# Kernel tuning notes

Hardware: AMD Instinct MI355X
Metric: run time of the kernel (lower is better)

The kernel has to match this reference:

```python
import jax, jax.numpy as jnp
import numpy as np

# Mamba2 config (matches mamba_ssm.Mamba2 defaults used by the wrapper)
D_MODEL = 1024
D_STATE = 128
D_CONV = 4
EXPAND = 2
HEADDIM = 64
CHUNK = 256
D_INNER = EXPAND * D_MODEL            # 2048
NHEADS = D_INNER // HEADDIM           # 32
CONV_DIM = D_INNER + 2 * D_STATE      # 2304 (x, B, C share the causal conv)
D_IN_PROJ = 2 * D_INNER + 2 * D_STATE + NHEADS  # z, xBC, dt
EPS = 1e-5


def rmsnorm(x, w, eps=EPS):
    return x * jax.lax.rsqrt(jnp.mean(x * x, axis=-1, keepdims=True) + eps) * w


def setup_inputs() -> dict:
    key = jax.random.key(0)
    ks = jax.random.split(key, 8)
    B, L = 2, 2048
    def w(k, shape, sc=0.02):
        return jax.random.normal(k, shape, jnp.float32) * sc
    return {
        "x": jax.random.normal(ks[0], (B, L, D_MODEL), jnp.float32),
        "norm_w": jnp.ones((D_MODEL,), jnp.float32),
        "in_proj_w": w(ks[1], (D_IN_PROJ, D_MODEL)),
        "conv_w": w(ks[2], (CONV_DIM, 1, D_CONV), 0.2),   # depthwise kernel
        "conv_b": jnp.zeros((CONV_DIM,), jnp.float32),
        "dt_bias": w(ks[3], (NHEADS,), 1.0),
        "A_log": jnp.log(1.0 + 15.0 * jax.random.uniform(ks[4], (NHEADS,), jnp.float32)),
        "D": jnp.ones((NHEADS,), jnp.float32),
        "gnorm_w": jnp.ones((D_INNER,), jnp.float32),
        "out_proj_w": w(ks[5], (D_MODEL, D_INNER)),
    }


def _ssd(xd, a, Bm, Cm):
    """Chunked SSD scan (ssd_minimal_discrete).
    xd: (b,l,h,p) = x*dt ; a: (b,l,h) = dt*A ; Bm,Cm: (b,l,n) (ngroups=1)."""
    b, l, h, p = xd.shape
    n = Bm.shape[-1]
    nc = l // CHUNK
    xd = xd.reshape(b, nc, CHUNK, h, p)
    a = a.reshape(b, nc, CHUNK, h).transpose(0, 3, 1, 2)   # (b,h,nc,c)
    Bm = Bm.reshape(b, nc, CHUNK, n)
    Cm = Cm.reshape(b, nc, CHUNK, n)
    a_cs = jnp.cumsum(a, axis=-1)                           # (b,h,nc,c)
    # 1) intra-chunk: causal decay matrix L[t,s] = exp(sum_{s<i<=t} a_i)
    diff = a_cs[..., :, None] - a_cs[..., None, :]          # (b,h,nc,c,c)
    mask = jnp.tril(jnp.ones((CHUNK, CHUNK), bool))
    Lm = jnp.exp(jnp.where(mask, diff, 0.0)) * mask
    Y_diag = jnp.einsum("bcln,bcsn,bhcls,bcshp->bclhp", Cm, Bm, Lm, xd)
    # 2) per-chunk end states
    decay_states = jnp.exp(a_cs[..., -1:] - a_cs)           # (b,h,nc,c)
    states = jnp.einsum("bcln,bhcl,bclhp->bchpn", Bm, decay_states, xd)
    # 3) inter-chunk recurrence (vectorized segsum over the 8+1 chunk totals)
    tot = jnp.pad(a_cs[..., -1], ((0, 0), (0, 0), (1, 0)))  # (b,h,nc+1)
    tot_cs = jnp.cumsum(tot, axis=-1)
    dchunk = tot_cs[..., :, None] - tot_cs[..., None, :]    # (b,h,nc+1,nc+1)
    cmask = jnp.tril(jnp.ones((nc + 1, nc + 1), bool))
    dchunk = jnp.exp(jnp.where(cmask, dchunk, 0.0)) * cmask
    states = jnp.concatenate([jnp.zeros_like(states[:, :1]), states], axis=1)
    new_states = jnp.einsum("bhzc,bchpn->bzhpn", dchunk, states)
    init_states = new_states[:, :-1]                        # state entering each chunk
    # 4) state -> output contribution
    Y_off = jnp.einsum("bcln,bchpn,bhcl->bclhp", Cm, init_states, jnp.exp(a_cs))
    return (Y_diag + Y_off).reshape(b, l, h, p)


def reference(x, norm_w, in_proj_w, conv_w, conv_b, dt_bias, A_log, D, gnorm_w, out_proj_w):
    res = x
    u = rmsnorm(x, norm_w)
    zxbcdt = u @ in_proj_w.T                                # (b,l,d_in_proj)
    z, xBC, dt = jnp.split(zxbcdt, [D_INNER, D_INNER + CONV_DIM], axis=-1)
    # causal depthwise conv1d over (x,B,C), then SiLU
    xBC_t = jnp.pad(xBC.transpose(0, 2, 1), ((0, 0), (0, 0), (D_CONV - 1, 0)))
    conv = jax.lax.conv_general_dilated(
        xBC_t, conv_w, (1,), "VALID",
        dimension_numbers=("NCH", "OIH", "NCH"), feature_group_count=CONV_DIM)
    xBC = jax.nn.silu(conv.transpose(0, 2, 1) + conv_b)
    xs, Bm, Cm = jnp.split(xBC, [D_INNER, D_INNER + D_STATE], axis=-1)
    dt = jax.nn.softplus(dt + dt_bias)                      # (b,l,h)
    A = -jnp.exp(A_log)                                     # (h,)
    xh = xs.reshape(xs.shape[0], xs.shape[1], NHEADS, HEADDIM)
    y = _ssd(xh * dt[..., None], dt * A, Bm, Cm)
    y = y + D[None, None, :, None] * xh                     # skip term
    y = y.reshape(xs.shape)
    y = rmsnorm(y * jax.nn.silu(z), gnorm_w)                # gated RMSNorm
    return res + y @ out_proj_w.T
```

## Files before the change

kernel.cpp:

```cpp
#include <hip/hip_runtime.h>
#include <hip/hip_bf16.h>

typedef __hip_bfloat16 bf16_t;
typedef __attribute__((ext_vector_type(8))) short bfrag8;
typedef __attribute__((ext_vector_type(4))) float floatx4;

#define DM     1024
#define DI     2048
#define NHD    32
#define HD     64
#define DSTATE 128
#define CONVD  2304
#define NPROJ  4384
#define NPAD   4480
#define MR     4096
#define LL     2048
#define EPSF   1e-5f
#define PSTR   40
#define LOG2E  1.44269504088896f

__device__ __forceinline__ void gl_lds16(const void* g, void* l) {
  __builtin_amdgcn_global_load_lds((const __attribute__((address_space(1))) void*)g,
                                   (__attribute__((address_space(3))) void*)l, 16, 0, 0);
}
__device__ __forceinline__ unsigned pack_bf16_rn(float a, float b) {
  unsigned ua = (__float_as_uint(a) + 0x8000u) >> 16;
  unsigned ub = (__float_as_uint(b) + 0x8000u) >> 16;
  return ua | (ub << 16);
}
__device__ __forceinline__ unsigned short bf16u(float a) {
  return (unsigned short)((__float_as_uint(a) + 0x8000u) >> 16);
}
__device__ __forceinline__ float blo(unsigned u){ return __uint_as_float(u << 16); }
__device__ __forceinline__ float bhi(unsigned u){ return __uint_as_float(u & 0xffff0000u); }
__device__ __forceinline__ void unp8(uint4 u, float* v) {
  v[0]=blo(u.x); v[1]=bhi(u.x); v[2]=blo(u.y); v[3]=bhi(u.y);
  v[4]=blo(u.z); v[5]=bhi(u.z); v[6]=blo(u.w); v[7]=bhi(u.w);
}

__global__ void rms1_kernel(const float* __restrict__ x, const float* __restrict__ w,
                            bf16_t* __restrict__ ub) {
  int row = blockIdx.x, t = threadIdx.x;
  float4 v = ((const float4*)(x + (long)row * DM))[t];
  float ss = v.x*v.x + v.y*v.y + v.z*v.z + v.w*v.w;
#pragma unroll
  for (int off = 32; off > 0; off >>= 1) ss += __shfl_down(ss, off, 64);
  __shared__ float red[4];
  if ((t & 63) == 0) red[t >> 6] = ss;
  __syncthreads();
  float tot = red[0] + red[1] + red[2] + red[3];
  float rs = rsqrtf(tot * (1.f / DM) + EPSF);
  float4 wv = ((const float4*)w)[t];
  bf16_t* o = ub + (long)row * DM + t * 4;
  o[0] = __float2bfloat16(v.x * rs * wv.x);
  o[1] = __float2bfloat16(v.y * rs * wv.y);
  o[2] = __float2bfloat16(v.z * rs * wv.z);
  o[3] = __float2bfloat16(v.w * rs * wv.w);
}

#define W1CNT (NPAD * DM / 4)
#define W2CNT (DM * DI / 4)
__global__ void cvtw_kernel(const float* __restrict__ w1, const float* __restrict__ w2,
                            bf16_t* __restrict__ o1, bf16_t* __restrict__ o2) {
  int i4 = blockIdx.x * 256 + threadIdx.x;
  if (i4 < W1CNT) {
    int idx = i4 * 4;
    int row = idx >> 10;
    float4 v = make_float4(0.f, 0.f, 0.f, 0.f);
    if (row < NPROJ) v = *(const float4*)(w1 + idx);
    bf16_t* d = o1 + idx;
    d[0] = __float2bfloat16(v.x); d[1] = __float2bfloat16(v.y);
    d[2] = __float2bfloat16(v.z); d[3] = __float2bfloat16(v.w);
  } else {
    int idx = (i4 - W1CNT) * 4;
    float4 v = *(const float4*)(w2 + idx);
    bf16_t* d = o2 + idx;
    d[0] = __float2bfloat16(v.x); d[1] = __float2bfloat16(v.y);
    d[2] = __float2bfloat16(v.z); d[3] = __float2bfloat16(v.w);
  }
}

template<int TN, bool DO_RES, bool OUT_BF16>
__global__ __launch_bounds__(256) void gemm64_kernel(const bf16_t* __restrict__ A,
    const bf16_t* __restrict__ Bw, const float* __restrict__ resid,
    void* __restrict__ Cout, int N, int K) {
  __shared__ bf16_t As[128 * 64];
  __shared__ bf16_t Bs[TN * 64];
  const int tid = threadIdx.x;
  const int lane = tid & 63;
  const int wv = tid >> 6;
  const int l15 = lane & 15;
  const int l4 = lane >> 4;
  constexpr int MF = (TN == 128) ? 4 : 2;
  const int wm = (TN == 128) ? ((wv >> 1) << 6) : (wv << 5);
  const int wn = (TN == 128) ? ((wv & 1) << 6) : 0;
  const int tm = blockIdx.x << 7;
  const int tn = blockIdx.y * TN;

  floatx4 acc[MF][4];
#pragma unroll
  for (int i = 0; i < MF; i++)
#pragma unroll
    for (int j = 0; j < 4; j++) acc[i][j] = (floatx4){0.f, 0.f, 0.f, 0.f};

  const int r = tid >> 3;
  const int c8 = tid & 7;
  const int scol = ((c8 ^ (r & 7)) << 3);
  const bf16_t* Ag = A + (long)(tm + r) * K + scol;
  const bf16_t* Bg = Bw + (long)(tn + r) * K + scol;
  const int swz = l15 & 7;

  for (int k0 = 0; k0 < K; k0 += 64) {
#pragma unroll
    for (int q = 0; q < 4; q++)
      gl_lds16(Ag + (long)(q * 32) * K + k0, &As[q * 2048 + tid * 8]);
#pragma unroll
    for (int q = 0; q < TN / 32; q++)
      gl_lds16(Bg + (long)(q * 32) * K + k0, &Bs[q * 2048 + tid * 8]);
    __syncthreads();
#pragma unroll
    for (int kk = 0; kk < 2; kk++) {
      bfrag8 af[MF], bfr[4];
      const int ch = ((kk << 2) | l4) ^ swz;
#pragma unroll
      for (int j = 0; j < 4; j++)
        bfr[j] = *(const bfrag8*)&Bs[(wn + j * 16 + l15) * 64 + ch * 8];
#pragma unroll
      for (int i = 0; i < MF; i++)
        af[i] = *(const bfrag8*)&As[(wm + i * 16 + l15) * 64 + ch * 8];
#pragma unroll
      for (int i = 0; i < MF; i++)
#pragma unroll
        for (int j = 0; j < 4; j++)
          acc[i][j] = __builtin_amdgcn_mfma_f32_16x16x32_bf16(af[i], bfr[j], acc[i][j], 0, 0, 0);
    }
    __syncthreads();
  }
#pragma unroll
  for (int i = 0; i < MF; i++)
#pragma unroll
    for (int j = 0; j < 4; j++)
#pragma unroll
      for (int r2 = 0; r2 < 4; r2++) {
        int row = tm + wm + i * 16 + l4 * 4 + r2;
        int col = tn + wn + j * 16 + l15;
        float v = acc[i][j][r2];
        if (OUT_BF16) {
          ((bf16_t*)Cout)[(long)row * N + col] = __float2bfloat16(v);
        } else {
          if (DO_RES) v += resid[(long)row * N + col];
          ((float*)Cout)[(long)row * N + col] = v;
        }
      }
}

__global__ __launch_bounds__(256) void gemm_s_kernel(const bf16_t* __restrict__ Cmh,
                const bf16_t* __restrict__ Bmh, float* __restrict__ SL) {
  __shared__ bf16_t As[128 * 32];
  __shared__ bf16_t Bs[128 * 32];
  const int tid = threadIdx.x;
  const int lane = tid & 63;
  const int wv = tid >> 6;
  const int wm = (wv >> 1) << 6;
  const int wn = (wv & 1) << 6;
  const int bc = blockIdx.z;
  const int tm = blockIdx.x << 7;
  const int tn = blockIdx.y << 7;
  const int l15 = lane & 15;
  const int l4 = lane >> 4;
  floatx4 acc[4][4];
#pragma unroll
  for (int i = 0; i < 4; i++)
#pragma unroll
    for (int j = 0; j < 4; j++) acc[i][j] = (floatx4){0.f, 0.f, 0.f, 0.f};
  const int arow = tid >> 2;
  const int acol = (tid & 3) << 3;
  const bf16_t* Ag = Cmh + (long)bc * 256 * DSTATE + (long)(tm + arow) * DSTATE + acol;
  const bf16_t* Bg = Bmh + (long)bc * 256 * DSTATE + (long)(tn + arow) * DSTATE + acol;
  const long k64 = (long)64 * DSTATE;
  for (int k0 = 0; k0 < DSTATE; k0 += 32) {
    gl_lds16(Ag + k0, &As[tid * 8]);
    gl_lds16(Ag + k64 + k0, &As[2048 + tid * 8]);
    gl_lds16(Bg + k0, &Bs[tid * 8]);
    gl_lds16(Bg + k64 + k0, &Bs[2048 + tid * 8]);
    __syncthreads();
    bfrag8 af[4], bfr[4];
#pragma unroll
    for (int i = 0; i < 4; i++)
      af[i] = *(const bfrag8*)&As[(wm + i * 16 + l15) * 32 + l4 * 8];
#pragma unroll
    for (int j = 0; j < 4; j++)
      bfr[j] = *(const bfrag8*)&Bs[(wn + j * 16 + l15) * 32 + l4 * 8];
#pragma unroll
    for (int i = 0; i < 4; i++)
#pragma unroll
      for (int j = 0; j < 4; j++)
        acc[i][j] = __builtin_amdgcn_mfma_f32_16x16x32_bf16(af[i], bfr[j], acc[i][j], 0, 0, 0);
    __syncthreads();
  }
  float* Cb = SL + (long)bc * 65536;
#pragma unroll
  for (int i = 0; i < 4; i++)
#pragma unroll
    for (int j = 0; j < 4; j++)
#pragma unroll
      for (int r = 0; r < 4; r++)
        Cb[(long)(tm + wm + i * 16 + l4 * 4 + r) * 256 + tn + wn + j * 16 + l15] = acc[i][j][r];
}

__global__ __launch_bounds__(256) void conv4_kernel(const bf16_t* __restrict__ zxh,
    const float* __restrict__ cw, const float* __restrict__ cb,
    bf16_t* __restrict__ xhb, bf16_t* __restrict__ Bmh, bf16_t* __restrict__ Cmh) {
  int g = blockIdx.x * 256 + threadIdx.x;
  int cg = g % 288;
  int blt = g / 288;
  int c0 = cg * 8;
  long bl0 = (long)blt * 4;
  int l0 = (int)(bl0 & (LL - 1));
  const bf16_t* base = zxh + bl0 * NPAD + DI + c0;
  float rv[7][8];
#pragma unroll
  for (int j = 0; j < 7; j++) {
    int dj = j - 3;
    if (l0 + dj >= 0) {
      uint4 u = *(const uint4*)(base + (long)dj * NPAD);
      unp8(u, rv[j]);
    } else {
#pragma unroll
      for (int q = 0; q < 8; q++) rv[j][q] = 0.f;
    }
  }
  float4 wq[8];
#pragma unroll
  for (int q = 0; q < 8; q++) wq[q] = ((const float4*)cw)[c0 + q];
  float bias[8];
  *(float4*)&bias[0] = *(const float4*)(cb + c0);
  *(float4*)&bias[4] = *(const float4*)(cb + c0 + 4);
#pragma unroll
  for (int i = 0; i < 4; i++) {
    unsigned o[4];
#pragma unroll
    for (int q2 = 0; q2 < 4; q2++) {
      float rr[2];
#pragma unroll
      for (int e = 0; e < 2; e++) {
        int q = q2 * 2 + e;
        float a = bias[q] + wq[q].x * rv[i][q] + wq[q].y * rv[i + 1][q]
                + wq[q].z * rv[i + 2][q] + wq[q].w * rv[i + 3][q];
        rr[e] = a / (1.f + __expf(-a));
      }
      o[q2] = pack_bf16_rn(rr[0], rr[1]);
    }
    uint4 ov = make_uint4(o[0], o[1], o[2], o[3]);
    long bl = bl0 + i;
    if (c0 < DI)               *(uint4*)(xhb + bl * DI + c0) = ov;
    else if (c0 < DI + DSTATE) *(uint4*)(Bmh + bl * DSTATE + (c0 - DI)) = ov;
    else                       *(uint4*)(Cmh + bl * DSTATE + (c0 - DI - DSTATE)) = ov;
  }
}

__global__ void acs_kernel(const bf16_t* __restrict__ zxh, const float* __restrict__ A_log,
                           const float* __restrict__ dtb,
                           float* __restrict__ acs, float* __restrict__ ctot,
                           float* __restrict__ dtout) {
  int blk = blockIdx.x;
  int h = blk & 31, bc = blk >> 5;
  int t = threadIdx.x, lane = t & 63, w = t >> 6;
  float Ah = -__expf(A_log[h]) * LOG2E;
  int gl = bc * 256 + t;
  float vv = __bfloat162float(zxh[(long)gl * NPAD + (NPROJ - 32) + h]) + dtb[h];
  float sp = fmaxf(vv, 0.f) + log1pf(__expf(-fabsf(vv)));
  dtout[gl * 32 + h] = sp;
  float a = sp * Ah;
#pragma unroll
  for (int off = 1; off < 64; off <<= 1) {
    float v = __shfl_up(a, off, 64);
    if (lane >= off) a += v;
  }
  __shared__ float wsum[4];
  if (lane == 63) wsum[w] = a;
  __syncthreads();
  float base = 0.f;
  for (int i = 0; i < 4; i++) base += (i < w) ? wsum[i] : 0.f;
  a += base;
  acs[blk * 256 + t] = a;
  if (t == 255) ctot[blk] = a;
}

__global__ __launch_bounds__(256) void xdt_kernel(const bf16_t* __restrict__ xhb,
    const bf16_t* __restrict__ Bmh, const float* __restrict__ dt,
    const float* __restrict__ acs, bf16_t* __restrict__ xdT,
    bf16_t* __restrict__ xdTe, bf16_t* __restrict__ BmT) {
  __shared__ unsigned short Tb[9216];
  int blk = blockIdx.x;
  int t = threadIdx.x;
  if (blk < 512) {
    unsigned short* T1 = Tb;
    unsigned short* T2 = Tb + 4608;
    int h = blk & 31, bc = blk >> 5;
    float atot = acs[blk * 256 + 255];
    int l_loc = t >> 2, pg = t & 3;
    for (int lt = 0; lt < 4; lt++) {
      int gl = bc * 256 + lt * 64 + l_loc;
      float w1 = dt[gl * 32 + h];
      float w2 = w1 * exp2f(atot - acs[blk * 256 + lt * 64 + l_loc]);
      const uint4* src = (const uint4*)(xhb + (long)gl * DI + h * HD + pg * 16);
      uint4 u0 = src[0], u1 = src[1];
      float v[16];
      unp8(u0, v); unp8(u1, v + 8);
      __syncthreads();
#pragma unroll
      for (int q = 0; q < 16; q++) {
        T1[(pg * 16 + q) * 72 + l_loc] = bf16u(v[q] * w1);
        T2[(pg * 16 + q) * 72 + l_loc] = bf16u(v[q] * w2);
      }
      __syncthreads();
      long orow = ((long)blk * 64 + l_loc) * 256 + lt * 64 + pg * 16;
      *(uint4*)(xdT + orow)      = *(uint4*)&T1[l_loc * 72 + pg * 16];
      *(uint4*)(xdT + orow + 8)  = *(uint4*)&T1[l_loc * 72 + pg * 16 + 8];
      *(uint4*)(xdTe + orow)     = *(uint4*)&T2[l_loc * 72 + pg * 16];
      *(uint4*)(xdTe + orow + 8) = *(uint4*)&T2[l_loc * 72 + pg * 16 + 8];
    }
  } else {
    unsigned short* T = Tb;
    int bc = blk - 512;
    int l_loc = t >> 2, ng = t & 3;
    for (int lt = 0; lt < 4; lt++) {
      int gl = bc * 256 + lt * 64 + l_loc;
      const uint4* src = (const uint4*)(Bmh + (long)gl * DSTATE + ng * 32);
      uint4 u[4];
#pragma unroll
      for (int q = 0; q < 4; q++) u[q] = src[q];
      __syncthreads();
      const unsigned short* us = (const unsigned short*)u;
#pragma unroll
      for (int e = 0; e < 32; e++)
        T[(ng * 32 + e) * 72 + l_loc] = us[e];
      __syncthreads();
      int n = t >> 1, lg2 = t & 1;
      long orow = ((long)bc * 128 + n) * 256 + lt * 64 + lg2 * 32;
#pragma unroll
      for (int q = 0; q < 4; q++)
        *(uint4*)(BmT + orow + q * 8) = *(uint4*)&T[n * 72 + lg2 * 32 + q * 8];
    }
  }
}

__global__ __launch_bounds__(256) void states3_kernel(const bf16_t* __restrict__ xdTe,
    const bf16_t* __restrict__ BmT, bf16_t* __restrict__ states) {
  int blk = blockIdx.x;
  int bc = blk >> 5;
  int t = threadIdx.x, lane = t & 63, wv = t >> 6;
  int l15 = lane & 15, l4 = lane >> 4;
  floatx4 acc[2][4];
#pragma unroll
  for (int i = 0; i < 2; i++)
#pragma unroll
    for (int j = 0; j < 4; j++) acc[i][j] = (floatx4){0.f, 0.f, 0.f, 0.f};
  const bf16_t* arow = BmT + (long)bc * 128 * 256;
  const bf16_t* brow = xdTe + (long)blk * 64 * 256;
#pragma unroll
  for (int kt = 0; kt < 8; kt++) {
    bfrag8 af[2], bfr[4];
#pragma unroll
    for (int i = 0; i < 2; i++)
      af[i] = *(const bfrag8*)(arow + (long)(wv * 32 + i * 16 + l15) * 256 + kt * 32 + l4 * 8);
#pragma unroll
    for (int j = 0; j < 4; j++)
      bfr[j] = *(const bfrag8*)(brow + (long)(j * 16 + l15) * 256 + kt * 32 + l4 * 8);
#pragma unroll
    for (int i = 0; i < 2; i++)
#pragma unroll
      for (int j = 0; j < 4; j++)
        acc[i][j] = __builtin_amdgcn_mfma_f32_16x16x32_bf16(af[i], bfr[j], acc[i][j], 0, 0, 0);
  }
#pragma unroll
  for (int i = 0; i < 2; i++)
#pragma unroll
    for (int j = 0; j < 4; j++) {
      int n_base = wv * 32 + i * 16 + l4 * 4;
      int p = j * 16 + l15;
      unsigned lo = pack_bf16_rn(acc[i][j][0], acc[i][j][1]);
      unsigned hi = pack_bf16_rn(acc[i][j][2], acc[i][j][3]);
      *(uint2*)(states + (long)blk * 8192 + p * 128 + n_base) = make_uint2(lo, hi);
    }
}

__global__ void scan_kernel(const bf16_t* __restrict__ states, const float* __restrict__ ctot,
                            bf16_t* __restrict__ initsb) {
  int id = blockIdx.x * 256 + threadIdx.x;
  int pn = id & 8191;
  int bh = id >> 13;
  int b = bh >> 5, h = bh & 31;
  float S = 0.f;
#pragma unroll
  for (int c = 0; c < 8; c++) {
    int blk = (b * 8 + c) * 32 + h;
    initsb[(long)blk * 8192 + pn] = __float2bfloat16(S);
    S = exp2f(ctot[blk]) * S + __bfloat162float(states[(long)blk * 8192 + pn]);
  }
}

__global__ __launch_bounds__(256) void yk3_kernel(const float* __restrict__ SL,
     const bf16_t* __restrict__ Cmh, const bf16_t* __restrict__ xhb,
     const bf16_t* __restrict__ zxh, const float* __restrict__ acs,
     const bf16_t* __restrict__ initsb, const bf16_t* __restrict__ xdT,
     const float* __restrict__ Dp, bf16_t* __restrict__ yg, float* __restrict__ ssqp) {
  int bi = blockIdx.x;
  int mh = bi & 1, h = (bi >> 1) & 31, bc = bi >> 6;
  int ablk = bc * 32 + h;
  int t = threadIdx.x;
  int lane = t & 63, wv = t >> 6;
  int l15 = lane & 15, l4 = lane >> 4;
  __shared__ float acsS[256];
  __shared__ bf16_t Ps[128 * PSTR];
  __shared__ __align__(16) char bbuf[49152];
  bf16_t* xds = (bf16_t*)bbuf;
  bf16_t* ins = (bf16_t*)(bbuf + 32768);
  float* Yt = (float*)bbuf;

  {
    const bf16_t* xrow_g = xdT + (long)ablk * 64 * 256;
#pragma unroll
    for (int it = 0; it < 8; it++) {
      int sl = it * 256 + t;
      int p = sl >> 5, s = sl & 31;
      int c = (s & 24) | ((s & 7) ^ (p & 7));
      gl_lds16(xrow_g + p * 256 + c * 8, &xds[sl * 8]);
    }
    const bf16_t* irow_g = initsb + (long)ablk * 8192;
#pragma unroll
    for (int it = 0; it < 4; it++) {
      int sl = it * 256 + t;
      int p = sl >> 4, s = sl & 15;
      int c = (s & 8) | ((s & 7) ^ (p & 7));
      gl_lds16(irow_g + p * 128 + c * 8, &ins[sl * 8]);
    }
  }
  acsS[t] = acs[ablk * 256 + t];
  __syncthreads();

  const int l_loc = t >> 1, half = t & 1;
  const int l = mh * 128 + l_loc;
  const float al = acsS[l];
  const float eAl = exp2f(al);
  const int rowbase = bc * 256;
  const float* SLb = SL + (long)bc * 65536 + (long)l * 256;

  floatx4 acc[2][4];
#pragma unroll
  for (int i = 0; i < 2; i++)
#pragma unroll
    for (int j = 0; j < 4; j++) acc[i][j] = (floatx4){0.f, 0.f, 0.f, 0.f};

  const int nkd = (mh + 1) * 4;
  float4 slv[4];
#pragma unroll
  for (int q = 0; q < 4; q++) slv[q] = ((const float4*)(SLb + half * 16))[q];

  for (int kt = 0; kt < nkd + 4; kt++) {
    unsigned pk[8];
    if (kt < nkd) {
      int s0 = kt * 32 + half * 16;
#pragma unroll
      for (int q = 0; q < 4; q++) {
        float4 v = slv[q];
        int sb = s0 + q * 4;
        float p0 = (sb + 0 <= l) ? v.x * exp2f(al - acsS[sb + 0]) : 0.f;
        float p1 = (sb + 1 <= l) ? v.y * exp2f(al - acsS[sb + 1]) : 0.f;
        float p2 = (sb + 2 <= l) ? v.z * exp2f(al - acsS[sb + 2]) : 0.f;
        float p3 = (sb + 3 <= l) ? v.w * exp2f(al - acsS[sb + 3]) : 0.f;
        pk[q * 2 + 0] = pack_bf16_rn(p0, p1);
        pk[q * 2 + 1] = pack_bf16_rn(p2, p3);
      }
    } else {
      int n0 = (kt - nkd) * 32;
      const uint4* Cg = (const uint4*)(Cmh + (long)(rowbase + l) * DSTATE + n0 + half * 16);
      uint4 u0 = Cg[0], u1 = Cg[1];
      float cv[16];
      unp8(u0, cv); unp8(u1, cv + 8);
#pragma unroll
      for (int q = 0; q < 8; q++)
        pk[q] = pack_bf16_rn(cv[q * 2] * eAl, cv[q * 2 + 1] * eAl);
    }
    {
      uint4* pw = (uint4*)&Ps[l_loc * PSTR + half * 16];
      pw[0] = make_uint4(pk[0], pk[1], pk[2], pk[3]);
      pw[1] = make_uint4(pk[4], pk[5], pk[6], pk[7]);
    }
    if (kt + 1 < nkd) {
#pragma unroll
      for (int q = 0; q < 4; q++)
        slv[q] = ((const float4*)(SLb + (kt + 1) * 32 + half * 16))[q];
    }
    __syncthreads();
    bfrag8 bfr[4];
    if (kt < nkd) {
      int ch = kt * 4 + l4;
#pragma unroll
      for (int j = 0; j < 4; j++) {
        int p = j * 16 + l15;
        int sw = (ch & 24) | ((ch & 7) ^ (p & 7));
        bfr[j] = *(const bfrag8*)&xds[(p * 32 + sw) * 8];
      }
    } else {
      int ch = (kt - nkd) * 4 + l4;
#pragma unroll
      for (int j = 0; j < 4; j++) {
        int p = j * 16 + l15;
        int sw = (ch & 8) | ((ch & 7) ^ (p & 7));
        bfr[j] = *(const bfrag8*)&ins[(p * 16 + sw) * 8];
      }
    }
#pragma unroll
    for (int i = 0; i < 2; i++) {
      bfrag8 af = *(const bfrag8*)&Ps[(wv * 32 + i * 16 + l15) * PSTR + l4 * 8];
#pragma unroll
      for (int j = 0; j < 4; j++)
        acc[i][j] = __builtin_amdgcn_mfma_f32_16x16x32_bf16(af, bfr[j], acc[i][j], 0, 0, 0);
    }
    __syncthreads();
  }
#pragma unroll
  for (int i = 0; i < 2; i++)
#pragma unroll
    for (int j = 0; j < 4; j++)
#pragma unroll
      for (int r = 0; r < 4; r++)
        Yt[(wv * 32 + i * 16 + l4 * 4 + r) * 66 + j * 16 + l15] = acc[i][j][r];
  __syncthreads();
  {
    int row_l = t >> 1;
    int ch = (t & 1) * 32;
    long rowg = rowbase + mh * 128 + row_l;
    float Dh = Dp[h];
    float ss = 0.f;
#pragma unroll
    for (int it = 0; it < 4; it++) {
      int c = ch + it * 8;
      float4 y0 = *(const float4*)&Yt[row_l * 66 + c];
      float4 y1 = *(const float4*)&Yt[row_l * 66 + c + 4];
      uint4 ux = *(const uint4*)(xhb + rowg * DI + h * HD + c);
      uint4 uz = *(const uint4*)(zxh + rowg * NPAD + h * HD + c);
      float xv[8], zv[8];
      unp8(ux, xv); unp8(uz, zv);
      float yv[8] = {y0.x, y0.y, y0.z, y0.w, y1.x, y1.y, y1.z, y1.w};
      unsigned o[4];
#pragma unroll
      for (int q = 0; q < 4; q++) {
        float v0 = (yv[q * 2 + 0] + Dh * xv[q * 2 + 0]) *
                   (zv[q * 2 + 0] / (1.f + __expf(-zv[q * 2 + 0])));
        float v1 = (yv[q * 2 + 1] + Dh * xv[q * 2 + 1]) *
                   (zv[q * 2 + 1] / (1.f + __expf(-zv[q * 2 + 1])));
        ss += v0 * v0 + v1 * v1;
        o[q] = pack_bf16_rn(v0, v1);
      }
      *(uint4*)(yg + rowg * DI + h * HD + c) = make_uint4(o[0], o[1], o[2], o[3]);
    }
    ss += __shfl_xor(ss, 1, 64);
    if ((t & 1) == 0) ssqp[rowg * 32 + h] = ss;
  }
}

__global__ void gnorm2_kernel(const bf16_t* __restrict__ yg, const float* __restrict__ ssqp,
                              const float* __restrict__ gw, bf16_t* __restrict__ yn) {
  int row = blockIdx.x, t = threadIdx.x;
  __shared__ float rsS;
  if (t < 64) {
    float v = (t < 32) ? ssqp[row * 32 + t] : 0.f;
#pragma unroll
    for (int off = 16; off > 0; off >>= 1) v += __shfl_down(v, off, 64);
    if (t == 0) rsS = rsqrtf(v * (1.f / DI) + EPSF);
  }
  __syncthreads();
  float rs = rsS;
  uint4 u = *(const uint4*)(yg + (long)row * DI + t * 8);
  float4 g0 = ((const float4*)gw)[t * 2];
  float4 g1 = ((const float4*)gw)[t * 2 + 1];
  unsigned o0 = pack_bf16_rn(blo(u.x) * rs * g0.x, bhi(u.x) * rs * g0.y);
  unsigned o1 = pack_bf16_rn(blo(u.y) * rs * g0.z, bhi(u.y) * rs * g0.w);
  unsigned o2 = pack_bf16_rn(blo(u.z) * rs * g1.x, bhi(u.z) * rs * g1.y);
  unsigned o3 = pack_bf16_rn(blo(u.w) * rs * g1.z, bhi(u.w) * rs * g1.w);
  *(uint4*)(yn + (long)row * DI + t * 8) = make_uint4(o0, o1, o2, o3);
}

extern "C" void kernel_launch(void* const* d_in, const int* in_sizes, int n_in,
                              void* d_out, int out_size, void* d_ws, size_t ws_size,
                              hipStream_t stream) {
  const float* x    = (const float*)d_in[0];
  const float* nw   = (const float*)d_in[1];
  const float* w1   = (const float*)d_in[2];
  const float* cw   = (const float*)d_in[3];
  const float* cb   = (const float*)d_in[4];
  const float* dtb  = (const float*)d_in[5];
  const float* alog = (const float*)d_in[6];
  const float* Dp   = (const float*)d_in[7];
  const float* gw   = (const float*)d_in[8];
  const float* w2   = (const float*)d_in[9];
  float* out = (float*)d_out;

  char* ws = (char*)d_ws;
  size_t off = 0;
  auto alloc = [&](size_t bytes) -> void* {
    void* p = ws + off;
    off += (bytes + 255) & ~(size_t)255;
    return p;
  };
  bf16_t* ub     = (bf16_t*)alloc((size_t)MR * DM * 2);
  bf16_t* w1b    = (bf16_t*)alloc((size_t)NPAD * DM * 2);
  bf16_t* w2b    = (bf16_t*)alloc((size_t)DM * DI * 2);
  bf16_t* zxh    = (bf16_t*)alloc((size_t)MR * NPAD * 2);
  bf16_t* xhb    = (bf16_t*)alloc((size_t)MR * DI * 2);
  bf16_t* Bmh    = (bf16_t*)alloc((size_t)MR * DSTATE * 2);
  bf16_t* Cmh    = (bf16_t*)alloc((size_t)MR * DSTATE * 2);
  float* SL      = (float*)alloc((size_t)16 * 256 * 256 * 4);
  float* dt      = (float*)alloc((size_t)MR * NHD * 4);
  float* acs     = (float*)alloc((size_t)512 * 256 * 4);
  float* ctot    = (float*)alloc((size_t)512 * 4);
  bf16_t* states = (bf16_t*)alloc((size_t)512 * 8192 * 2);
  bf16_t* initsb = (bf16_t*)alloc((size_t)512 * 8192 * 2);
  bf16_t* xdT    = (bf16_t*)alloc((size_t)512 * 64 * 256 * 2);
  bf16_t* xdTe   = (bf16_t*)alloc((size_t)512 * 64 * 256 * 2);
  bf16_t* BmT    = (bf16_t*)alloc((size_t)16 * 128 * 256 * 2);
  bf16_t* yg     = (bf16_t*)alloc((size_t)MR * DI * 2);
  float* ssqp    = (float*)alloc((size_t)MR * NHD * 4);
  bf16_t* yn     = (bf16_t*)alloc((size_t)MR * DI * 2);
  if (off > ws_size) return;

  rms1_kernel<<<MR, 256, 0, stream>>>(x, nw, ub);
  cvtw_kernel<<<(W1CNT + W2CNT) / 256, 256, 0, stream>>>(w1, w2, w1b, w2b);
  gemm64_kernel<128, false, true><<<dim3(MR / 128, NPAD / 128), 256, 0, stream>>>(
      ub, w1b, nullptr, zxh, NPAD, DM);
  conv4_kernel<<<(1024 * 288) / 256, 256, 0, stream>>>(zxh, cw, cb, xhb, Bmh, Cmh);
  acs_kernel<<<512, 256, 0, stream>>>(zxh, alog, dtb, acs, ctot, dt);
  xdt_kernel<<<528, 256, 0, stream>>>(xhb, Bmh, dt, acs, xdT, xdTe, BmT);
  gemm_s_kernel<<<dim3(2, 2, 16), 256, 0, stream>>>(Cmh, Bmh, SL);
  states3_kernel<<<512, 256, 0, stream>>>(xdTe, BmT, states);
  scan_kernel<<<(2 * 32 * 8192) / 256, 256, 0, stream>>>(states, ctot, initsb);
  yk3_kernel<<<1024, 256, 0, stream>>>(SL, Cmh, xhb, zxh, acs, initsb, xdT, Dp, yg, ssqp);
  gnorm2_kernel<<<MR, 256, 0, stream>>>(yg, ssqp, gw, yn);
  gemm64_kernel<64, true, false><<<dim3(MR / 128, DM / 64), 256, 0, stream>>>(
      yn, w2b, x, out, DM, DI);
}
```

Measured before the change: 290.6 us.

## Fold gated RMSNorm into out-proj GEMM epilogue and merge acs into xdt

The gnorm weight is folded into the bf16 out_proj weight during conversion. The per-row rsqrt scale is applied in the final GEMM epilogue, so the full normalized activation tensor is no longer written and re-read, and a small reduction kernel now computes the per-row scales. Separately, the dt softplus and cumulative-sum computation is moved into the xdt kernel and kept in shared memory, which removes one launch and the dt buffer. A side effect is that the GEMM now consumes unrounded yg values scaled after accumulation, which changes bf16 rounding slightly.

```diff
diff --git a/kernel.cpp b/kernel.cpp
--- a/kernel.cpp
+++ b/kernel.cpp
@@ -61,6 +61,7 @@
 #define W1CNT (NPAD * DM / 4)
 #define W2CNT (DM * DI / 4)
 __global__ void cvtw_kernel(const float* __restrict__ w1, const float* __restrict__ w2,
+                            const float* __restrict__ gw,
                             bf16_t* __restrict__ o1, bf16_t* __restrict__ o2) {
   int i4 = blockIdx.x * 256 + threadIdx.x;
   if (i4 < W1CNT) {
@@ -73,17 +74,19 @@
     d[2] = __float2bfloat16(v.z); d[3] = __float2bfloat16(v.w);
   } else {
     int idx = (i4 - W1CNT) * 4;
+    int k = idx & (DI - 1);
     float4 v = *(const float4*)(w2 + idx);
+    float4 g = *(const float4*)(gw + k);
     bf16_t* d = o2 + idx;
-    d[0] = __float2bfloat16(v.x); d[1] = __float2bfloat16(v.y);
-    d[2] = __float2bfloat16(v.z); d[3] = __float2bfloat16(v.w);
+    d[0] = __float2bfloat16(v.x * g.x); d[1] = __float2bfloat16(v.y * g.y);
+    d[2] = __float2bfloat16(v.z * g.z); d[3] = __float2bfloat16(v.w * g.w);
   }
 }
 
 template<int TN, bool DO_RES, bool OUT_BF16>
 __global__ __launch_bounds__(256) void gemm64_kernel(const bf16_t* __restrict__ A,
     const bf16_t* __restrict__ Bw, const float* __restrict__ resid,
-    void* __restrict__ Cout, int N, int K) {
+    const float* __restrict__ rs_row, void* __restrict__ Cout, int N, int K) {
   __shared__ bf16_t As[128 * 64];
   __shared__ bf16_t Bs[TN * 64];
   const int tid = threadIdx.x;
@@ -148,7 +151,7 @@
         if (OUT_BF16) {
           ((bf16_t*)Cout)[(long)row * N + col] = __float2bfloat16(v);
         } else {
-          if (DO_RES) v += resid[(long)row * N + col];
+          if (DO_RES) v = v * rs_row[row] + resid[(long)row * N + col];
           ((float*)Cout)[(long)row * N + col] = v;
         }
       }
@@ -259,51 +262,51 @@
   }
 }
 
-__global__ void acs_kernel(const bf16_t* __restrict__ zxh, const float* __restrict__ A_log,
-                           const float* __restrict__ dtb,
-                           float* __restrict__ acs, float* __restrict__ ctot,
-                           float* __restrict__ dtout) {
-  int blk = blockIdx.x;
-  int h = blk & 31, bc = blk >> 5;
-  int t = threadIdx.x, lane = t & 63, w = t >> 6;
-  float Ah = -__expf(A_log[h]) * LOG2E;
-  int gl = bc * 256 + t;
-  float vv = __bfloat162float(zxh[(long)gl * NPAD + (NPROJ - 32) + h]) + dtb[h];
-  float sp = fmaxf(vv, 0.f) + log1pf(__expf(-fabsf(vv)));
-  dtout[gl * 32 + h] = sp;
-  float a = sp * Ah;
-#pragma unroll
-  for (int off = 1; off < 64; off <<= 1) {
-    float v = __shfl_up(a, off, 64);
-    if (lane >= off) a += v;
-  }
+__global__ __launch_bounds__(256) void xdt_kernel(const bf16_t* __restrict__ xhb,
+    const bf16_t* __restrict__ Bmh, const bf16_t* __restrict__ zxh,
+    const float* __restrict__ A_log, const float* __restrict__ dtb,
+    float* __restrict__ acs, float* __restrict__ ctot,
+    bf16_t* __restrict__ xdT, bf16_t* __restrict__ xdTe, bf16_t* __restrict__ BmT) {
+  __shared__ unsigned short Tb[9216];
+  __shared__ float acsL[256];
+  __shared__ float dtsL[256];
   __shared__ float wsum[4];
-  if (lane == 63) wsum[w] = a;
-  __syncthreads();
-  float base = 0.f;
-  for (int i = 0; i < 4; i++) base += (i < w) ? wsum[i] : 0.f;
-  a += base;
-  acs[blk * 256 + t] = a;
-  if (t == 255) ctot[blk] = a;
-}
-
-__global__ __launch_bounds__(256) void xdt_kernel(const bf16_t* __restrict__ xhb,
-    const bf16_t* __restrict__ Bmh, const float* __restrict__ dt,
-    const float* __restrict__ acs, bf16_t* __restrict__ xdT,
-    bf16_t* __restrict__ xdTe, bf16_t* __restrict__ BmT) {
-  __shared__ unsigned short Tb[9216];
   int blk = blockIdx.x;
   int t = threadIdx.x;
   if (blk < 512) {
+    int h = blk & 31, bc = blk >> 5;
+    {
+      int lane = t & 63, w = t >> 6;
+      float Ah = -__expf(A_log[h]) * LOG2E;
+      int gl = bc * 256 + t;
+      float vv = __bfloat162float(zxh[(long)gl * NPAD + (NPROJ - 32) + h]) + dtb[h];
+      float sp = fmaxf(vv, 0.f) + log1pf(__expf(-fabsf(vv)));
+      float a = sp * Ah;
+#pragma unroll
+      for (int off = 1; off < 64; off <<= 1) {
+        float v = __shfl_up(a, off, 64);
+        if (lane >= off) a += v;
+      }
+      if (lane == 63) wsum[w] = a;
+      __syncthreads();
+      float base = 0.f;
+      for (int i = 0; i < 4; i++) base += (i < w) ? wsum[i] : 0.f;
+      a += base;
+      acsL[t] = a;
+      dtsL[t] = sp;
+      acs[blk * 256 + t] = a;
+      if (t == 255) ctot[blk] = a;
+      __syncthreads();
+    }
+    float atot = acsL[255];
     unsigned short* T1 = Tb;
     unsigned short* T2 = Tb + 4608;
-    int h = blk & 31, bc = blk >> 5;
-    float atot = acs[blk * 256 + 255];
     int l_loc = t >> 2, pg = t & 3;
     for (int lt = 0; lt < 4; lt++) {
-      int gl = bc * 256 + lt * 64 + l_loc;
-      float w1 = dt[gl * 32 + h];
-      float w2 = w1 * exp2f(atot - acs[blk * 256 + lt * 64 + l_loc]);
+      int ll = lt * 64 + l_loc;
+      int gl = bc * 256 + ll;
+      float w1 = dtsL[ll];
+      float w2 = w1 * exp2f(atot - acsL[ll]);
       const uint4* src = (const uint4*)(xhb + (long)gl * DI + h * HD + pg * 16);
       uint4 u0 = src[0], u1 = src[1];
       float v[16];
@@ -562,26 +565,16 @@
   }
 }
 
-__global__ void gnorm2_kernel(const bf16_t* __restrict__ yg, const float* __restrict__ ssqp,
-                              const float* __restrict__ gw, bf16_t* __restrict__ yn) {
-  int row = blockIdx.x, t = threadIdx.x;
-  __shared__ float rsS;
-  if (t < 64) {
-    float v = (t < 32) ? ssqp[row * 32 + t] : 0.f;
-#pragma unroll
-    for (int off = 16; off > 0; off >>= 1) v += __shfl_down(v, off, 64);
-    if (t == 0) rsS = rsqrtf(v * (1.f / DI) + EPSF);
-  }
-  __syncthreads();
-  float rs = rsS;
-  uint4 u = *(const uint4*)(yg + (long)row * DI + t * 8);
-  float4 g0 = ((const float4*)gw)[t * 2];
-  float4 g1 = ((const float4*)gw)[t * 2 + 1];
-  unsigned o0 = pack_bf16_rn(blo(u.x) * rs * g0.x, bhi(u.x) * rs * g0.y);
-  unsigned o1 = pack_bf16_rn(blo(u.y) * rs * g0.z, bhi(u.y) * rs * g0.w);
-  unsigned o2 = pack_bf16_rn(blo(u.z) * rs * g1.x, bhi(u.z) * rs * g1.y);
-  unsigned o3 = pack_bf16_rn(blo(u.w) * rs * g1.z, bhi(u.w) * rs * g1.w);
-  *(uint4*)(yn + (long)row * DI + t * 8) = make_uint4(o0, o1, o2, o3);
+__global__ void rsred_kernel(const float* __restrict__ ssqp, float* __restrict__ rs) {
+  int row = blockIdx.x * 256 + threadIdx.x;
+  const float4* p = (const float4*)(ssqp + row * 32);
+  float s = 0.f;
+#pragma unroll
+  for (int q = 0; q < 8; q++) {
+    float4 v = p[q];
+    s += v.x + v.y + v.z + v.w;
+  }
+  rs[row] = rsqrtf(s * (1.f / DI) + EPSF);
 }
 
 extern "C" void kernel_launch(void* const* d_in, const int* in_sizes, int n_in,
@@ -614,7 +607,6 @@
   bf16_t* Bmh    = (bf16_t*)alloc((size_t)MR * DSTATE * 2);
   bf16_t* Cmh    = (bf16_t*)alloc((size_t)MR * DSTATE * 2);
   float* SL      = (float*)alloc((size_t)16 * 256 * 256 * 4);
-  float* dt      = (float*)alloc((size_t)MR * NHD * 4);
   float* acs     = (float*)alloc((size_t)512 * 256 * 4);
   float* ctot    = (float*)alloc((size_t)512 * 4);
   bf16_t* states = (bf16_t*)alloc((size_t)512 * 8192 * 2);
@@ -624,21 +616,20 @@
   bf16_t* BmT    = (bf16_t*)alloc((size_t)16 * 128 * 256 * 2);
   bf16_t* yg     = (bf16_t*)alloc((size_t)MR * DI * 2);
   float* ssqp    = (float*)alloc((size_t)MR * NHD * 4);
-  bf16_t* yn     = (bf16_t*)alloc((size_t)MR * DI * 2);
+  float* rs      = (float*)alloc((size_t)MR * 4);
   if (off > ws_size) return;
 
   rms1_kernel<<<MR, 256, 0, stream>>>(x, nw, ub);
-  cvtw_kernel<<<(W1CNT + W2CNT) / 256, 256, 0, stream>>>(w1, w2, w1b, w2b);
+  cvtw_kernel<<<(W1CNT + W2CNT) / 256, 256, 0, stream>>>(w1, w2, gw, w1b, w2b);
   gemm64_kernel<128, false, true><<<dim3(MR / 128, NPAD / 128), 256, 0, stream>>>(
-      ub, w1b, nullptr, zxh, NPAD, DM);
+      ub, w1b, nullptr, nullptr, zxh, NPAD, DM);
   conv4_kernel<<<(1024 * 288) / 256, 256, 0, stream>>>(zxh, cw, cb, xhb, Bmh, Cmh);
-  acs_kernel<<<512, 256, 0, stream>>>(zxh, alog, dtb, acs, ctot, dt);
-  xdt_kernel<<<528, 256, 0, stream>>>(xhb, Bmh, dt, acs, xdT, xdTe, BmT);
+  xdt_kernel<<<528, 256, 0, stream>>>(xhb, Bmh, zxh, alog, dtb, acs, ctot, xdT, xdTe, BmT);
   gemm_s_kernel<<<dim3(2, 2, 16), 256, 0, stream>>>(Cmh, Bmh, SL);
   states3_kernel<<<512, 256, 0, stream>>>(xdTe, BmT, states);
   scan_kernel<<<(2 * 32 * 8192) / 256, 256, 0, stream>>>(states, ctot, initsb);
   yk3_kernel<<<1024, 256, 0, stream>>>(SL, Cmh, xhb, zxh, acs, initsb, xdT, Dp, yg, ssqp);
-  gnorm2_kernel<<<MR, 256, 0, stream>>>(yg, ssqp, gw, yn);
+  rsred_kernel<<<MR / 256, 256, 0, stream>>>(ssqp, rs);
   gemm64_kernel<64, true, false><<<dim3(MR / 128, DM / 64), 256, 0, stream>>>(
-      yn, w2b, x, out, DM, DI);
-}
+      yg, w2b, x, rs, out, DM, DI);
+}
```

Result: faster. 282.7 us (-2.7%).
